# Performance work log

Hardware: AMD Instinct MI355X
Metric: run time of the kernel (lower is better)

## Reference

```python
import jax, jax.numpy as jnp
import numpy as np

I, H, O = 8, 32, 1  # input_size, hidden_size, output_size


def setup_inputs() -> dict:
    key = jax.random.key(0)
    ks = jax.random.split(key, 7)
    B, T = 4096, 256
    s_ih = 1.0 / np.sqrt(H)
    inp = {
        "x": jax.random.normal(ks[0], (B, T, I), dtype=jnp.float32),
        # PyTorch nn.LSTM params, gate order [i, f, g, o]
        "W_ih": jax.random.uniform(ks[1], (4 * H, I), minval=-s_ih, maxval=s_ih, dtype=jnp.float32),
        "W_hh": jax.random.uniform(ks[2], (4 * H, H), minval=-s_ih, maxval=s_ih, dtype=jnp.float32),
        "b_ih": jax.random.uniform(ks[3], (4 * H,), minval=-s_ih, maxval=s_ih, dtype=jnp.float32),
        "b_hh": jax.random.uniform(ks[4], (4 * H,), minval=-s_ih, maxval=s_ih, dtype=jnp.float32),
        # nn.Linear(H, O)
        "W_out": jax.random.uniform(ks[5], (O, H), minval=-s_ih, maxval=s_ih, dtype=jnp.float32),
        "b_out": jax.random.uniform(ks[6], (O,), minval=-s_ih, maxval=s_ih, dtype=jnp.float32),
    }
    return inp


def _lstm_last_h(x, W_ih, W_hh, b_ih, b_hh):
    B = x.shape[0]
    # Precompute input projections for all steps: [T, B, 4H]
    x_proj = jnp.einsum("bti,gi->tbg", x, W_ih) + (b_ih + b_hh)
    h0 = jnp.zeros((B, H), dtype=x.dtype)
    c0 = jnp.zeros((B, H), dtype=x.dtype)

    def step(carry, xp):
        h, c = carry
        z = xp + h @ W_hh.T  # [B, 4H]
        i = jax.nn.sigmoid(z[:, 0 * H:1 * H])
        f = jax.nn.sigmoid(z[:, 1 * H:2 * H])
        g = jnp.tanh(z[:, 2 * H:3 * H])
        o = jax.nn.sigmoid(z[:, 3 * H:4 * H])
        c = f * c + i * g
        h = o * jnp.tanh(c)
        return (h, c), None

    (hT, _), _ = jax.lax.scan(step, (h0, c0), x_proj)
    return hT  # equals out[:, -1, :] for unidirectional batch_first LSTM


def reference(x, W_ih, W_hh, b_ih, b_hh, W_out, b_out):
    hT = _lstm_last_h(x, W_ih, W_hh, b_ih, b_hh)
    return hT @ W_out.T + b_out  # [B, O]
```

## Files before the change

### kernel.cpp

```cpp
#include <hip/hip_runtime.h>


#define T_LEN   256
#define HALF_T  128
#define XSTRIDE 130
#define LOG2E   1.4426950408889634f

typedef short bf16x8 __attribute__((ext_vector_type(8)));
typedef float f32x4  __attribute__((ext_vector_type(4)));
typedef unsigned u32x4 __attribute__((ext_vector_type(4)));

static __device__ inline short f2bf_rne(float f) {
    union { float f; unsigned u; } v; v.f = f;
    unsigned u = v.u;
    return (short)((u + 0x7FFFu + ((u >> 16) & 1u)) >> 16);
}
static __device__ inline short f2bf_fast(float f) {
    union { float f; unsigned u; } v; v.f = f;
    return (short)((v.u + 0x8000u) >> 16);
}
static __device__ inline unsigned pack_bf2(float a, float b) {
    union { float f; unsigned u; } x, y; x.f = a; y.f = b;
    return ((x.u + 0x8000u) >> 16) | ((y.u + 0x8000u) & 0xFFFF0000u);
}
static __device__ inline float bf2f(short s) {
    union { unsigned u; float f; } v;
    v.u = ((unsigned)(unsigned short)s) << 16;
    return v.f;
}

__global__ __launch_bounds__(512, 2) void lstm_kernel(
    const float* __restrict__ x, const float* __restrict__ W_ih,
    const float* __restrict__ W_hh, const float* __restrict__ b_ih,
    const float* __restrict__ b_hh, const float* __restrict__ W_out,
    const float* __restrict__ b_out, float* __restrict__ out)
{
    __shared__ __attribute__((aligned(16))) short xl[HALF_T * XSTRIDE];
    __shared__ __attribute__((aligned(16))) short h_lds[2][16 * 40];

    const int tid  = threadIdx.x;
    const int w    = tid >> 6;
    const int lane = tid & 63;
    const int L    = lane & 15;
    const int q    = lane >> 4;
    const int row0 = blockIdx.x * 16;
    const float4* xv = (const float4*)x;

    const int   n  = 32 * (L & 3) + 4 * w + (L >> 2);
    const float sc = ((L & 3) == 2 ? 2.f * LOG2E : LOG2E);
    bf16x8 whh_f, wih_f = (bf16x8){0,0,0,0,0,0,0,0};
    {
        const float* src = W_hh + n * 32 + q * 8;
#pragma unroll
        for (int j = 0; j < 8; ++j) whh_f[j] = f2bf_rne(src[j] * sc);
        if (q == 0) {
            const float* s2 = W_ih + n * 8;
#pragma unroll
            for (int j = 0; j < 8; ++j) wih_f[j] = f2bf_rne(s2[j] * sc);
        }
    }
    f32x4 bias;
#pragma unroll
    for (int r = 0; r < 4; ++r) {
        const int   nr = 32 * r + 4 * w + q;
        const float sr = (r == 2 ? 2.f * LOG2E : LOG2E);
        bias[r] = (b_ih[nr] + b_hh[nr]) * sr;
    }

    for (int i = tid; i < 16 * 40; i += 512) h_lds[0][i] = 0;

#pragma unroll
    for (int it = 0; it < 4; ++it) {
        const int idx = tid + (it << 9);
        const int L2  = idx >> 7;
        const int tl  = idx & (HALF_T - 1);
        const float4* srcp = xv + ((size_t)(row0 + L2) * T_LEN + tl) * 2;
        const float4 a = srcp[0], b = srcp[1];
        u32x4 u;
        u[0] = pack_bf2(a.x, a.y); u[1] = pack_bf2(a.z, a.w);
        u[2] = pack_bf2(b.x, b.y); u[3] = pack_bf2(b.z, b.w);
        *(u32x4*)(&xl[tl * XSTRIDE + L2 * 8]) = u;
    }
    __syncthreads();

    f32x4 zx;
    {
        const bf16x8 xf0 = *(const bf16x8*)(&xl[L * 8]);
        zx = __builtin_amdgcn_mfma_f32_16x16x32_bf16(wih_f, xf0, bias, 0, 0, 0);
    }

    float c = 0.f;
    const int hw_off = 4 * w + q;

#pragma unroll 2
    for (int t = 0; t < T_LEN; ++t) {
        if (t == HALF_T - 1) {
#pragma unroll
            for (int it = 0; it < 4; ++it) {
                const int idx = tid + (it << 9);
                const int L2  = idx >> 7;
                const int tl  = idx & (HALF_T - 1);
                const float4* srcp = xv + ((size_t)(row0 + L2) * T_LEN + HALF_T + tl) * 2;
                const float4 a = srcp[0], b = srcp[1];
                u32x4 u;
                u[0] = pack_bf2(a.x, a.y); u[1] = pack_bf2(a.z, a.w);
                u[2] = pack_bf2(b.x, b.y); u[3] = pack_bf2(b.z, b.w);
                *(u32x4*)(&xl[tl * XSTRIDE + L2 * 8]) = u;
            }
            __syncthreads();
        }

        const int par = t & 1, nxt = par ^ 1;

        const bf16x8 hfrag = *(const bf16x8*)(&h_lds[par][L * 40 + q * 8]);
        int tn = t + 1; if (tn >= T_LEN) tn = T_LEN - 1;
        const bf16x8 xfrag = *(const bf16x8*)(&xl[(tn & (HALF_T - 1)) * XSTRIDE + L * 8]);

        const f32x4 acc = __builtin_amdgcn_mfma_f32_16x16x32_bf16(whh_f, hfrag, zx, 0, 0, 0);
        zx = __builtin_amdgcn_mfma_f32_16x16x32_bf16(wih_f, xfrag, bias, 0, 0, 0);

        {
            const float ei = __builtin_amdgcn_exp2f(-acc[0]);
            const float ef = __builtin_amdgcn_exp2f(-acc[1]);
            const float eg = __builtin_amdgcn_exp2f(-acc[2]);
            const float eo = __builtin_amdgcn_exp2f(-acc[3]);
            const float fv = __builtin_amdgcn_rcpf(1.f + ef);
            const float ig = (1.f - eg) * __builtin_amdgcn_rcpf((1.f + ei) * (1.f + eg));
            c = fmaf(fv, c, ig);
            const float ec = __builtin_amdgcn_exp2f(fminf(c * (-2.f * LOG2E), 40.f));
            const float hv = (1.f - ec) * __builtin_amdgcn_rcpf((1.f + eo) * (1.f + ec));
            h_lds[nxt][L * 40 + hw_off] = f2bf_fast(hv);
        }

        __syncthreads();
    }

    if (tid < 16) {
        float s = b_out[0];
#pragma unroll
        for (int k = 0; k < 32; ++k) s = fmaf(bf2f(h_lds[0][tid * 40 + k]), W_out[k], s);
        out[row0 + tid] = s;
    }
}

extern "C" void kernel_launch(void* const* d_in, const int* in_sizes, int n_in,
                              void* d_out, int out_size, void* d_ws, size_t ws_size,
                              hipStream_t stream) {
    const float* x     = (const float*)d_in[0];
    const float* W_ih  = (const float*)d_in[1];
    const float* W_hh  = (const float*)d_in[2];
    const float* b_ih  = (const float*)d_in[3];
    const float* b_hh  = (const float*)d_in[4];
    const float* W_out = (const float*)d_in[5];
    const float* b_out = (const float*)d_in[6];
    float* out = (float*)d_out;

    const int B = in_sizes[0] / (T_LEN * 8);
    const int tiles = B / 16;
    lstm_kernel<<<tiles, 512, 0, stream>>>(x, W_ih, W_hh, b_ih, b_hh, W_out, b_out, out);
}
```

Before: 141.4 us.

## Replace block barrier with per-wave LDS step flags and register-prefetch x

Each step's __syncthreads is replaced by a spin-wait on per-wave step counters in LDS. Each wave publishes its step after its h store completes, so waves can run up to one step apart. The x input is no longer staged through a large LDS tile; each lane keeps a 4-deep register ring of future timesteps loaded straight from global memory. This removes the mid-sequence reload barrier and shrinks LDS use, at the cost of polling overhead, extra VGPRs and small strided global loads on the critical loop.

```diff
diff --git a/kernel.cpp b/kernel.cpp
--- a/kernel.cpp
+++ b/kernel.cpp
@@ -1,14 +1,12 @@
 #include <hip/hip_runtime.h>
 
 
-#define T_LEN   256
-#define HALF_T  128
-#define XSTRIDE 130
-#define LOG2E   1.4426950408889634f
+#define T_LEN 256
+#define LOG2E 1.4426950408889634f
+#define WAIT_LGKM0 0xC07F
 
 typedef short bf16x8 __attribute__((ext_vector_type(8)));
 typedef float f32x4  __attribute__((ext_vector_type(4)));
-typedef unsigned u32x4 __attribute__((ext_vector_type(4)));
 
 static __device__ inline short f2bf_rne(float f) {
     union { float f; unsigned u; } v; v.f = f;
@@ -35,8 +33,8 @@
     const float* __restrict__ b_hh, const float* __restrict__ W_out,
     const float* __restrict__ b_out, float* __restrict__ out)
 {
-    __shared__ __attribute__((aligned(16))) short xl[HALF_T * XSTRIDE];
     __shared__ __attribute__((aligned(16))) short h_lds[2][16 * 40];
+    __shared__ unsigned wstep[8];
 
     const int tid  = threadIdx.x;
     const int w    = tid >> 6;
@@ -44,7 +42,6 @@
     const int L    = lane & 15;
     const int q    = lane >> 4;
     const int row0 = blockIdx.x * 16;
-    const float4* xv = (const float4*)x;
 
     const int   n  = 32 * (L & 3) + 4 * w + (L >> 2);
     const float sc = ((L & 3) == 2 ? 2.f * LOG2E : LOG2E);
@@ -68,56 +65,52 @@
     }
 
     for (int i = tid; i < 16 * 40; i += 512) h_lds[0][i] = 0;
+    if (tid < 8) wstep[tid] = 0;
+    __syncthreads();
 
-#pragma unroll
-    for (int it = 0; it < 4; ++it) {
-        const int idx = tid + (it << 9);
-        const int L2  = idx >> 7;
-        const int tl  = idx & (HALF_T - 1);
-        const float4* srcp = xv + ((size_t)(row0 + L2) * T_LEN + tl) * 2;
-        const float4 a = srcp[0], b = srcp[1];
-        u32x4 u;
-        u[0] = pack_bf2(a.x, a.y); u[1] = pack_bf2(a.z, a.w);
-        u[2] = pack_bf2(b.x, b.y); u[3] = pack_bf2(b.z, b.w);
-        *(u32x4*)(&xl[tl * XSTRIDE + L2 * 8]) = u;
-    }
-    __syncthreads();
+    const float4* xv = (const float4*)x;
+    const size_t  xb = (size_t)(row0 + L) * (T_LEN * 8 / 4);
+    float4 r0[4], r1[4];
+    const float4 a0 = xv[xb + 0], b0 = xv[xb + 1];
+    r0[1] = xv[xb + 2]; r1[1] = xv[xb + 3];
+    r0[2] = xv[xb + 4]; r1[2] = xv[xb + 5];
+    r0[3] = xv[xb + 6]; r1[3] = xv[xb + 7];
+    r0[0] = xv[xb + 8]; r1[0] = xv[xb + 9];
 
     f32x4 zx;
     {
-        const bf16x8 xf0 = *(const bf16x8*)(&xl[L * 8]);
-        zx = __builtin_amdgcn_mfma_f32_16x16x32_bf16(wih_f, xf0, bias, 0, 0, 0);
+        unsigned uu[4];
+        uu[0] = pack_bf2(a0.x, a0.y); uu[1] = pack_bf2(a0.z, a0.w);
+        uu[2] = pack_bf2(b0.x, b0.y); uu[3] = pack_bf2(b0.z, b0.w);
+        zx = __builtin_amdgcn_mfma_f32_16x16x32_bf16(wih_f, *(const bf16x8*)uu, bias, 0, 0, 0);
     }
 
     float c = 0.f;
-    const int hw_off = 4 * w + q;
+    const int hr = L * 40 + q * 8;
+    const int hw = L * 40 + 4 * w + q;
+    volatile unsigned* wsp = &wstep[lane & 7];
 
 #pragma unroll 2
     for (int t = 0; t < T_LEN; ++t) {
-        if (t == HALF_T - 1) {
-#pragma unroll
-            for (int it = 0; it < 4; ++it) {
-                const int idx = tid + (it << 9);
-                const int L2  = idx >> 7;
-                const int tl  = idx & (HALF_T - 1);
-                const float4* srcp = xv + ((size_t)(row0 + L2) * T_LEN + HALF_T + tl) * 2;
-                const float4 a = srcp[0], b = srcp[1];
-                u32x4 u;
-                u[0] = pack_bf2(a.x, a.y); u[1] = pack_bf2(a.z, a.w);
-                u[2] = pack_bf2(b.x, b.y); u[3] = pack_bf2(b.z, b.w);
-                *(u32x4*)(&xl[tl * XSTRIDE + L2 * 8]) = u;
-            }
-            __syncthreads();
-        }
+        while (!__all(*wsp >= (unsigned)t)) {}
+        asm volatile("" ::: "memory");
 
-        const int par = t & 1, nxt = par ^ 1;
-
-        const bf16x8 hfrag = *(const bf16x8*)(&h_lds[par][L * 40 + q * 8]);
-        int tn = t + 1; if (tn >= T_LEN) tn = T_LEN - 1;
-        const bf16x8 xfrag = *(const bf16x8*)(&xl[(tn & (HALF_T - 1)) * XSTRIDE + L * 8]);
+        const int par = t & 1;
+        const bf16x8 hfrag = *(const bf16x8*)(&h_lds[par][hr]);
 
         const f32x4 acc = __builtin_amdgcn_mfma_f32_16x16x32_bf16(whh_f, hfrag, zx, 0, 0, 0);
-        zx = __builtin_amdgcn_mfma_f32_16x16x32_bf16(wih_f, xfrag, bias, 0, 0, 0);
+
+        {
+            const int s = (t + 1) & 3;
+            const float4 a = r0[s], b = r1[s];
+            unsigned uu[4];
+            uu[0] = pack_bf2(a.x, a.y); uu[1] = pack_bf2(a.z, a.w);
+            uu[2] = pack_bf2(b.x, b.y); uu[3] = pack_bf2(b.z, b.w);
+            zx = __builtin_amdgcn_mfma_f32_16x16x32_bf16(wih_f, *(const bf16x8*)uu, bias, 0, 0, 0);
+            int tn = t + 5; if (tn >= T_LEN) tn = T_LEN - 1;
+            r0[s] = xv[xb + (size_t)tn * 2];
+            r1[s] = xv[xb + (size_t)tn * 2 + 1];
+        }
 
         {
             const float ei = __builtin_amdgcn_exp2f(-acc[0]);
@@ -129,12 +122,17 @@
             c = fmaf(fv, c, ig);
             const float ec = __builtin_amdgcn_exp2f(fminf(c * (-2.f * LOG2E), 40.f));
             const float hv = (1.f - ec) * __builtin_amdgcn_rcpf((1.f + eo) * (1.f + ec));
-            h_lds[nxt][L * 40 + hw_off] = f2bf_fast(hv);
+            h_lds[par ^ 1][hw] = f2bf_fast(hv);
         }
 
-        __syncthreads();
+        asm volatile("" ::: "memory");
+        __builtin_amdgcn_s_waitcnt(WAIT_LGKM0);
+        if (lane == 0) *(volatile unsigned*)&wstep[w] = (unsigned)(t + 1);
+        asm volatile("" ::: "memory");
     }
 
+    while (!__all(*wsp >= (unsigned)T_LEN)) {}
+    asm volatile("" ::: "memory");
     if (tid < 16) {
         float s = b_out[0];
 #pragma unroll
```

Measured after the change: 326.2 us. 2.31x slower.
